# Optimization experiments

Measured on AMD Instinct MI355X. Metric: run time of the kernel, lower is better.

The kernel has to match this reference:

```python
import jax, jax.numpy as jnp
import numpy as np

P = 7            # pooling_size
SCALE = 1.0 / 16  # spatial_scale


def _roi_align(feat, tf):
    # feat: [B,C,T,H,W] (L2-normalized), tf: [N,7] = [b, x1, y1, t1, x2, y2, t2]
    # RoIAlignAvg with temporal pooled size == T (identity in time): bilinear
    # sample at each spatial bin center for every frame.
    H, W = feat.shape[-2], feat.shape[-1]
    b = tf[:, 0].astype(jnp.int32)
    x1, y1 = tf[:, 1] * SCALE, tf[:, 2] * SCALE
    x2, y2 = tf[:, 4] * SCALE, tf[:, 5] * SCALE
    bw = jnp.maximum(x2 - x1 + SCALE, 1e-3) / P
    bh = jnp.maximum(y2 - y1 + SCALE, 1e-3) / P
    ctr = jnp.arange(P, dtype=feat.dtype) + 0.5
    xs = jnp.clip(x1[:, None] + ctr * bw[:, None], 0.0, W - 1)  # [N,P]
    ys = jnp.clip(y1[:, None] + ctr * bh[:, None], 0.0, H - 1)  # [N,P]
    x0 = jnp.floor(xs); y0 = jnp.floor(ys)
    fx = xs - x0; fy = ys - y0
    x0i = x0.astype(jnp.int32); x1i = jnp.minimum(x0i + 1, W - 1)
    y0i = y0.astype(jnp.int32); y1i = jnp.minimum(y0i + 1, H - 1)

    def g(yi, xi):
        # advanced indices broadcast to [N,P,P]; result [N,P,P,C,T]
        return feat[b[:, None, None], :, :, yi[:, :, None], xi[:, None, :]]

    wy0 = (1 - fy)[:, :, None, None, None]; wy1 = fy[:, :, None, None, None]
    wx0 = (1 - fx)[:, None, :, None, None]; wx1 = fx[:, None, :, None, None]
    out = (wy0 * wx0 * g(y0i, x0i) + wy0 * wx1 * g(y0i, x1i)
           + wy1 * wx0 * g(y1i, x0i) + wy1 * wx1 * g(y1i, x1i))
    return jnp.transpose(out, (0, 3, 4, 1, 2))  # [N,C,T,P,P]


def _forward(base_feat, tubes, gt_rois, gt_tubes, conv_w, conv_b, w1, b1, w2, b2, wp, bp):
    B, C, T = base_feat.shape[:3]
    R = tubes.shape[1]
    # F.normalize(base_feat, p=2, dim=1)
    feat = base_feat / jnp.maximum(
        jnp.linalg.norm(base_feat, axis=1, keepdims=True), 1e-12)

    # --- ragged scatter: rois[b,i,t1:t2+1,1:] = tubes[b,i,[1,2,4,5]] ---
    f = jnp.arange(T)
    f_off = (f[None, :] + jnp.arange(B)[:, None] * T).astype(tubes.dtype)  # [B,T]
    t1 = tubes[..., 3].astype(jnp.int32)[..., None]
    t2 = tubes[..., 6].astype(jnp.int32)[..., None]
    mask = (f[None, None, :] >= t1) & (f[None, None, :] <= t2)  # [B,R,T]
    box = tubes[..., jnp.array([1, 2, 4, 5])]                   # [B,R,4]
    rois_box = jnp.where(mask[..., None], box[:, :, None, :],
                         jnp.zeros((), tubes.dtype))
    rois = jnp.concatenate(
        [jnp.broadcast_to(f_off[:, None, :, None], (B, R, T, 1)), rois_box], -1)

    # --- RoIAlign + AvgPool3d over T + head (eval mode: dropout = identity) ---
    pooled = _roi_align(feat, tubes.reshape(-1, 7))  # [N,C,T,P,P]
    pooled = pooled.mean(axis=2)                     # [N,C,P,P]
    x = jnp.einsum('nchw,oc->nohw', pooled, conv_w) + conv_b[None, :, None, None]
    x = x.reshape(x.shape[0], -1)                    # [N, C*P*P]
    x = jax.nn.relu(x @ w1 + b1)
    x = jax.nn.relu(x @ w2 + b2)
    bbox_pred = x @ wp + bp                          # [N, 4*T]
    return bbox_pred, pooled, rois


def setup_inputs() -> dict:
    B, R, T, C, HF, IMG = 4, 64, 16, 256, 14, 224
    ks = jax.random.split(jax.random.key(0), 16)
    base_feat = jax.random.normal(ks[0], (B, C, T, HF, HF), jnp.float32)
    x1 = jax.random.uniform(ks[1], (B, R), minval=0.0, maxval=IMG / 2)
    y1 = jax.random.uniform(ks[2], (B, R), minval=0.0, maxval=IMG / 2)
    x2 = jnp.minimum(x1 + jax.random.uniform(ks[3], (B, R), minval=16.0, maxval=IMG / 2), IMG - 1.0)
    y2 = jnp.minimum(y1 + jax.random.uniform(ks[4], (B, R), minval=16.0, maxval=IMG / 2), IMG - 1.0)
    tt = jax.random.randint(ks[5], (B, R, 2), 0, T)
    t1 = jnp.min(tt, -1).astype(jnp.float32)
    t2 = jnp.max(tt, -1).astype(jnp.float32)
    bidx = jnp.broadcast_to(jnp.arange(B)[:, None], (B, R)).astype(jnp.float32)
    tubes = jnp.stack([bidx, x1, y1, t1, x2, y2, t2], -1)
    s = 0.02
    return {
        'base_feat': base_feat,
        'tubes': tubes,
        'gt_rois': jax.random.normal(ks[6], (B, 10, T, 5), jnp.float32),
        'gt_tubes': jax.random.normal(ks[7], (B, 10, 7), jnp.float32),
        'conv_w': jax.random.normal(ks[8], (C, C), jnp.float32) * s,
        'conv_b': jnp.zeros((C,), jnp.float32),
        'w1': jax.random.normal(ks[9], (C * P * P, 2048), jnp.float32) * s,
        'b1': jnp.zeros((2048,), jnp.float32),
        'w2': jax.random.normal(ks[10], (2048, 512), jnp.float32) * s,
        'b2': jnp.zeros((512,), jnp.float32),
        'wp': jax.random.normal(ks[11], (512, 4 * T), jnp.float32) * s,
        'bp': jnp.zeros((4 * T,), jnp.float32),
    }


def reference(base_feat, tubes, gt_rois, gt_tubes, conv_w, conv_b, w1, b1, w2, b2, wp, bp):
    return _forward(base_feat, tubes, gt_rois, gt_tubes, conv_w, conv_b, w1, b1, w2, b2, wp, bp)
```

## Files before the change

### kernel.cpp

```cpp
#include <hip/hip_runtime.h>

#define HH 14
#define WW 14
#define HWSZ 196
#define TT 16
#define CC 256
#define BB 4
#define RR 64
#define NROI 256
#define PP 7
#define PP2 49

typedef short s4v __attribute__((ext_vector_type(4)));
typedef short s8v __attribute__((ext_vector_type(8)));
typedef float f4v __attribute__((ext_vector_type(4)));

__device__ inline ushort f2bf(float f) {
    union { float f; unsigned u; } v; v.f = f;
    unsigned r = v.u + 0x7fffu + ((v.u >> 16) & 1u);
    return (ushort)(r >> 16);
}
__device__ inline float bf2f(ushort u) {
    union { unsigned u; float f; } v; v.u = ((unsigned)u) << 16;
    return v.f;
}

__global__ void k_sumsq(const float* __restrict__ base, float* __restrict__ partial) {
    int blk = blockIdx.x;
    int bt = blk >> 3, cg = blk & 7;
    int hw = threadIdx.x;
    if (hw >= HWSZ) return;
    int b = bt >> 4, t = bt & 15;
    const float* p = base + ((size_t)(b * CC + cg * 32) * TT + t) * HWSZ + hw;
    float s = 0.f;
    #pragma unroll 8
    for (int c = 0; c < 32; ++c) {
        float v = p[(size_t)c * TT * HWSZ];
        s += v * v;
    }
    partial[cg * 12544 + bt * HWSZ + hw] = s;
}

__global__ void k_finish_inv(const float* __restrict__ partial, float* __restrict__ inv) {
    int j = blockIdx.x * 256 + threadIdx.x;
    if (j >= 12544) return;
    float s = 0.f;
    #pragma unroll
    for (int cg = 0; cg < 8; ++cg) s += partial[cg * 12544 + j];
    inv[j] = 1.0f / fmaxf(sqrtf(s), 1e-12f);
}

__global__ void k_tsum(const float* __restrict__ base, const float* __restrict__ inv,
                       float* __restrict__ tsum) {
    int bc = blockIdx.x;
    int hw = threadIdx.x;
    if (hw >= HWSZ) return;
    int b = bc >> 8;
    const float* p = base + (size_t)bc * TT * HWSZ + hw;
    const float* iv = inv + b * TT * HWSZ + hw;
    float s = 0.f;
    #pragma unroll
    for (int t = 0; t < TT; ++t) s += p[t * HWSZ] * iv[t * HWSZ];
    tsum[(size_t)bc * HWSZ + hw] = s;
}

__global__ void k_roialign(const float* __restrict__ tubes, const float* __restrict__ tsum,
                           float* __restrict__ pooled, float* __restrict__ pooledT,
                           float* __restrict__ rois) {
    __shared__ int sx0[PP], sx1[PP], sy0[PP], sy1[PP];
    __shared__ float sfx[PP], sfy[PP];
    __shared__ int sb;
    int n = blockIdx.x;
    int tid = threadIdx.x;
    if (tid < PP) {
        const float* tb = tubes + n * 7;
        float x1 = tb[1] * 0.0625f, y1 = tb[2] * 0.0625f;
        float x2 = tb[4] * 0.0625f, y2 = tb[5] * 0.0625f;
        float bw = fmaxf(x2 - x1 + 0.0625f, 0.001f) * (1.0f / PP);
        float bh = fmaxf(y2 - y1 + 0.0625f, 0.001f) * (1.0f / PP);
        float ctr = tid + 0.5f;
        float xs = fminf(fmaxf(x1 + ctr * bw, 0.f), (float)(WW - 1));
        float ys = fminf(fmaxf(y1 + ctr * bh, 0.f), (float)(HH - 1));
        float x0f = floorf(xs), y0f = floorf(ys);
        int x0 = (int)x0f, y0 = (int)y0f;
        sx0[tid] = x0; sx1[tid] = min(x0 + 1, WW - 1);
        sy0[tid] = y0; sy1[tid] = min(y0 + 1, HH - 1);
        sfx[tid] = xs - x0f; sfy[tid] = ys - y0f;
        if (tid == 0) sb = (int)tb[0];
    }
    if (tid < TT) {
        const float* tb = tubes + n * 7;
        int t1 = (int)tb[3], t2 = (int)tb[6];
        bool m = (tid >= t1) && (tid <= t2);
        int b = n >> 6;
        float* o = rois + ((size_t)n * TT + tid) * 5;
        o[0] = (float)(b * TT + tid);
        o[1] = m ? tb[1] : 0.f;
        o[2] = m ? tb[2] : 0.f;
        o[3] = m ? tb[4] : 0.f;
        o[4] = m ? tb[5] : 0.f;
    }
    __syncthreads();
    const float* tbase = tsum + (size_t)sb * CC * HWSZ;

    for (int idx = tid; idx < CC * PP2; idx += 256) {
        int c = idx / PP2, bin = idx - (idx / PP2) * PP2;
        int py = bin / PP, px = bin - (bin / PP) * PP;
        const float* tp = tbase + (size_t)c * HWSZ;
        float fx = sfx[px], fy = sfy[py];
        int y0 = sy0[py] * WW, y1 = sy1[py] * WW;
        float v00 = tp[y0 + sx0[px]];
        float v01 = tp[y0 + sx1[px]];
        float v10 = tp[y1 + sx0[px]];
        float v11 = tp[y1 + sx1[px]];
        float v = (1.f - fy) * ((1.f - fx) * v00 + fx * v01)
                + fy        * ((1.f - fx) * v10 + fx * v11);
        pooled[(size_t)n * CC * PP2 + idx] = v * (1.0f / TT);
    }
    for (int idx = tid; idx < PP2 * CC; idx += 256) {
        int bin = idx >> 8, c = idx & 255;
        int py = bin / PP, px = bin - (bin / PP) * PP;
        const float* tp = tbase + (size_t)c * HWSZ;
        float fx = sfx[px], fy = sfy[py];
        int y0 = sy0[py] * WW, y1 = sy1[py] * WW;
        float v00 = tp[y0 + sx0[px]];
        float v01 = tp[y0 + sx1[px]];
        float v10 = tp[y1 + sx0[px]];
        float v11 = tp[y1 + sx1[px]];
        float v = (1.f - fy) * ((1.f - fx) * v00 + fx * v01)
                + fy        * ((1.f - fx) * v10 + fx * v11);
        pooledT[((size_t)n * PP2 + bin) * CC + c] = v * (1.0f / TT);
    }
}

__global__ __launch_bounds__(512) void conv_mfma(const float* __restrict__ pooledT,
                                                 const float* __restrict__ conv_w,
                                                 const float* __restrict__ conv_b,
                                                 ushort* __restrict__ xb) {
    __shared__ __align__(16) ushort Ab[2][8192];
    __shared__ __align__(16) ushort Bres[8192];
    const int m0 = blockIdx.x * 256, o0 = blockIdx.y * 64;
    const int tid = threadIdx.x;
    const int lane = tid & 63, w = tid >> 6;
    const int wm = w & 3, wn = w >> 2;
    const int fr = lane & 15, fg = lane >> 4;

    for (int ii = tid; ii < 2048; ii += 512) {
        int o_l = ii >> 5, cq = ii & 31;
        const float* s = conv_w + (size_t)(o0 + o_l) * 256 + cq * 8;
        float4 v0 = *(const float4*)s;
        float4 v1 = *(const float4*)(s + 4);
        float vv[8] = {v0.x, v0.y, v0.z, v0.w, v1.x, v1.y, v1.z, v1.w};
        int dbase = (cq >> 2) * 2048 + (o_l >> 4) * 512 + (cq & 3) * 128 + (o_l & 15);
        #pragma unroll
        for (int jc = 0; jc < 8; ++jc) Bres[dbase + jc * 16] = f2bf(vv[jc]);
    }

    int ii0 = tid, ii1 = 512 + tid, ii2 = 1024 + tid, ii3 = 1536 + tid;
    const float* pA0 = pooledT + (size_t)(m0 + (ii0 >> 3)) * 256 + (ii0 & 7) * 4;
    const float* pA1 = pooledT + (size_t)(m0 + (ii1 >> 3)) * 256 + (ii1 & 7) * 4;
    const float* pA2 = pooledT + (size_t)(m0 + (ii2 >> 3)) * 256 + (ii2 & 7) * 4;
    const float* pA3 = pooledT + (size_t)(m0 + (ii3 >> 3)) * 256 + (ii3 & 7) * 4;
#define CDOFF(ii) (((ii >> 3) >> 4) * 512 + ((ii & 7) >> 1) * 128 + ((ii >> 3) & 15) * 8 + (ii & 1) * 4)
    const int do0 = CDOFF(ii0), do1 = CDOFF(ii1), do2 = CDOFF(ii2), do3 = CDOFF(ii3);
#undef CDOFF
    float4 a0_, a1_, a2_, a3_;
#define CONV_LOAD(t) do { a0_ = *(const float4*)(pA0 + (t) * 32); \
                          a1_ = *(const float4*)(pA1 + (t) * 32); \
                          a2_ = *(const float4*)(pA2 + (t) * 32); \
                          a3_ = *(const float4*)(pA3 + (t) * 32); } while (0)
#define W4(dst, v) do { s4v _u; _u[0]=(short)f2bf((v).x); _u[1]=(short)f2bf((v).y); \
                        _u[2]=(short)f2bf((v).z); _u[3]=(short)f2bf((v).w); \
                        *(s4v*)(dst) = _u; } while (0)
#define CONV_WRITE(buf) do { W4(Ab[buf] + do0, a0_); W4(Ab[buf] + do1, a1_); \
                             W4(Ab[buf] + do2, a2_); W4(Ab[buf] + do3, a3_); } while (0)

    CONV_LOAD(0);
    CONV_WRITE(0);
    __syncthreads();

    const int aoff = wm * 2048 + fg * 128 + fr * 8;
    f4v acc[4][2];
    #pragma unroll
    for (int i = 0; i < 4; ++i)
        #pragma unroll
        for (int j = 0; j < 2; ++j) acc[i][j] = (f4v){0.f, 0.f, 0.f, 0.f};

    for (int t = 0; t < 8; ++t) {
        if (t < 7) CONV_LOAD(t + 1);
        const ushort* A = Ab[t & 1];
        s8v a0 = *(const s8v*)(A + aoff);
        s8v a1 = *(const s8v*)(A + aoff + 512);
        s8v a2 = *(const s8v*)(A + aoff + 1024);
        s8v a3 = *(const s8v*)(A + aoff + 1536);
        unsigned bbase = (unsigned)(size_t)(&Bres[0]) + t * 4096 + wn * 2048 + fg * 256 + fr * 2;
        s4v bl0, bh0, bl1, bh1;
        asm volatile("ds_read_b64_tr_b16 %0, %2\n\t"
                     "ds_read_b64_tr_b16 %1, %2 offset:128"
                     : "=v"(bl0), "=v"(bh0) : "v"(bbase));
        asm volatile("ds_read_b64_tr_b16 %0, %2 offset:1024\n\t"
                     "ds_read_b64_tr_b16 %1, %2 offset:1152"
                     : "=v"(bl1), "=v"(bh1) : "v"(bbase));
        asm volatile("s_waitcnt lgkmcnt(0)" ::: "memory");
        __builtin_amdgcn_sched_barrier(0);
        s8v b0, b1;
        b0[0] = bl0[0]; b0[1] = bl0[1]; b0[2] = bl0[2]; b0[3] = bl0[3];
        b0[4] = bh0[0]; b0[5] = bh0[1]; b0[6] = bh0[2]; b0[7] = bh0[3];
        b1[0] = bl1[0]; b1[1] = bl1[1]; b1[2] = bl1[2]; b1[3] = bl1[3];
        b1[4] = bh1[0]; b1[5] = bh1[1]; b1[6] = bh1[2]; b1[7] = bh1[3];
        acc[0][0] = __builtin_amdgcn_mfma_f32_16x16x32_bf16(a0, b0, acc[0][0], 0, 0, 0);
        acc[0][1] = __builtin_amdgcn_mfma_f32_16x16x32_bf16(a0, b1, acc[0][1], 0, 0, 0);
        acc[1][0] = __builtin_amdgcn_mfma_f32_16x16x32_bf16(a1, b0, acc[1][0], 0, 0, 0);
        acc[1][1] = __builtin_amdgcn_mfma_f32_16x16x32_bf16(a1, b1, acc[1][1], 0, 0, 0);
        acc[2][0] = __builtin_amdgcn_mfma_f32_16x16x32_bf16(a2, b0, acc[2][0], 0, 0, 0);
        acc[2][1] = __builtin_amdgcn_mfma_f32_16x16x32_bf16(a2, b1, acc[2][1], 0, 0, 0);
        acc[3][0] = __builtin_amdgcn_mfma_f32_16x16x32_bf16(a3, b0, acc[3][0], 0, 0, 0);
        acc[3][1] = __builtin_amdgcn_mfma_f32_16x16x32_bf16(a3, b1, acc[3][1], 0, 0, 0);
        if (t < 7) CONV_WRITE((t + 1) & 1);
        __syncthreads();
    }
#undef CONV_LOAD
#undef CONV_WRITE
#undef W4

    #pragma unroll
    for (int ni = 0; ni < 2; ++ni) {
        int o = o0 + wn * 32 + ni * 16 + fr;
        float cb = conv_b[o];
        int obase = (o >> 5) * 8192 + (((o >> 3) & 3)) * 128 + (o & 7);
        #pragma unroll
        for (int mi = 0; mi < 4; ++mi)
            #pragma unroll
            for (int i = 0; i < 4; ++i) {
                int gm = m0 + wm * 64 + mi * 16 + fg * 4 + i;
                int n = gm / 49, hw = gm - n * 49;
                xb[(size_t)hw * 65536 + obase + (n >> 4) * 512 + (n & 15) * 8]
                    = f2bf(acc[mi][ni][i] + cb);
            }
    }
}

__global__ __launch_bounds__(512) void fc1_mfma(const ushort* __restrict__ xb,
                                                const float* __restrict__ w1,
                                                ushort* __restrict__ partb) {
    __shared__ __align__(16) ushort Ab[4][8192];
    __shared__ __align__(16) ushort Bbf[2][2048];
    const int s = blockIdx.x, nblk = blockIdx.y;
    const int n0 = nblk * 64;
    const int k0 = s * 1568;
    const int tid = threadIdx.x;
    const int lane = tid & 63, w = tid >> 6;
    const int wm = w & 3, wn = w >> 2;
    const int fr = lane & 15, fg = lane >> 4;

    const ushort* gA = xb + (size_t)s * 49 * 8192;
    const int slot0 = tid, slot1 = 512 + tid;

    const int kr = (w >> 2) * 16 + (lane >> 2);
    const int bnb = w & 3, bnq = lane & 3;
    const int ncol = n0 + bnb * 16 + bnq * 4;
    const int bw_u = bnb * 512 + kr * 16 + bnq * 4;

    const int aoff = wm * 2048 + fg * 128 + fr * 8;
    f4v acc[4][2];
    #pragma unroll
    for (int i = 0; i < 4; ++i)
        #pragma unroll
        for (int j = 0; j < 2; ++j) acc[i][j] = (f4v){0.f, 0.f, 0.f, 0.f};

#define STAGE_A(buf, kg) do {                                                                   \
    ushort* _d = Ab[buf];                                                                       \
    __builtin_amdgcn_global_load_lds(                                                           \
        (const __attribute__((address_space(1))) void*)(gA + (size_t)(kg) * 8192 + slot0 * 8),  \
        (__attribute__((address_space(3))) void*)(_d + slot0 * 8), 16, 0, 0);                   \
    __builtin_amdgcn_global_load_lds(                                                           \
        (const __attribute__((address_space(1))) void*)(gA + (size_t)(kg) * 8192 + slot1 * 8),  \
        (__attribute__((address_space(3))) void*)(_d + slot1 * 8), 16, 0, 0);                   \
} while (0)
#define GBP(t) (*(const float4*)(w1 +                                                           \
    (size_t)(((unsigned)(k0 + (t) * 32 + kr) & 255u) * 49 +                                     \
             ((unsigned)(k0 + (t) * 32 + kr) >> 8)) * 2048 + ncol))
#define BWRITE(buf, rb) do {                                                                    \
    s4v _u; _u[0] = (short)f2bf((rb).x); _u[1] = (short)f2bf((rb).y);                           \
    _u[2] = (short)f2bf((rb).z); _u[3] = (short)f2bf((rb).w);                                   \
    *(s4v*)&Bbf[buf][bw_u] = _u;                                                                \
} while (0)

    float4 rb0, rb1, rb2, rb3;
    STAGE_A(0, 0);
    STAGE_A(1, 1);
    rb0 = GBP(0); rb1 = GBP(1); rb2 = GBP(2); rb3 = GBP(3);
    BWRITE(0, rb0);
    __builtin_amdgcn_sched_barrier(0);
    asm volatile("s_waitcnt vmcnt(3) lgkmcnt(0)" ::: "memory");
    __builtin_amdgcn_s_barrier();
    __builtin_amdgcn_sched_barrier(0);

#define FC1_BODY(t, rbL, rbU) do {                                                              \
    int kg2 = (t) + 2 > 48 ? 48 : (t) + 2;                                                      \
    int kg4 = (t) + 4 > 48 ? 48 : (t) + 4;                                                      \
    STAGE_A(((t) + 2) & 3, kg2);                                                                \
    __builtin_amdgcn_sched_barrier(0);                                                          \
    rbL = GBP(kg4);                                                                             \
    __builtin_amdgcn_sched_barrier(0);                                                          \
    const ushort* _A = Ab[(t) & 3];                                                             \
    s8v _a0 = *(const s8v*)(_A + aoff);                                                         \
    s8v _a1 = *(const s8v*)(_A + aoff + 512);                                                   \
    s8v _a2 = *(const s8v*)(_A + aoff + 1024);                                                  \
    s8v _a3 = *(const s8v*)(_A + aoff + 1536);                                                  \
    unsigned _bb = (unsigned)(size_t)(&Bbf[(t) & 1][0]) + wn * 2048 + fg * 256 + fr * 2;        \
    s4v _bl0, _bh0, _bl1, _bh1;                                                                 \
    asm volatile("ds_read_b64_tr_b16 %0, %2\n\t"                                                \
                 "ds_read_b64_tr_b16 %1, %2 offset:128"                                         \
                 : "=v"(_bl0), "=v"(_bh0) : "v"(_bb));                                          \
    asm volatile("ds_read_b64_tr_b16 %0, %2 offset:1024\n\t"                                    \
                 "ds_read_b64_tr_b16 %1, %2 offset:1152"                                        \
                 : "=v"(_bl1), "=v"(_bh1) : "v"(_bb));                                          \
    asm volatile("s_waitcnt lgkmcnt(0)" ::: "memory");                                          \
    __builtin_amdgcn_sched_barrier(0);                                                          \
    s8v _b0, _b1;                                                                               \
    _b0[0]=_bl0[0]; _b0[1]=_bl0[1]; _b0[2]=_bl0[2]; _b0[3]=_bl0[3];                             \
    _b0[4]=_bh0[0]; _b0[5]=_bh0[1]; _b0[6]=_bh0[2]; _b0[7]=_bh0[3];                             \
    _b1[0]=_bl1[0]; _b1[1]=_bl1[1]; _b1[2]=_bl1[2]; _b1[3]=_bl1[3];                             \
    _b1[4]=_bh1[0]; _b1[5]=_bh1[1]; _b1[6]=_bh1[2]; _b1[7]=_bh1[3];                             \
    acc[0][0] = __builtin_amdgcn_mfma_f32_16x16x32_bf16(_a0, _b0, acc[0][0], 0, 0, 0);          \
    acc[0][1] = __builtin_amdgcn_mfma_f32_16x16x32_bf16(_a0, _b1, acc[0][1], 0, 0, 0);          \
    acc[1][0] = __builtin_amdgcn_mfma_f32_16x16x32_bf16(_a1, _b0, acc[1][0], 0, 0, 0);          \
    acc[1][1] = __builtin_amdgcn_mfma_f32_16x16x32_bf16(_a1, _b1, acc[1][1], 0, 0, 0);          \
    acc[2][0] = __builtin_amdgcn_mfma_f32_16x16x32_bf16(_a2, _b0, acc[2][0], 0, 0, 0);          \
    acc[2][1] = __builtin_amdgcn_mfma_f32_16x16x32_bf16(_a2, _b1, acc[2][1], 0, 0, 0);          \
    acc[3][0] = __builtin_amdgcn_mfma_f32_16x16x32_bf16(_a3, _b0, acc[3][0], 0, 0, 0);          \
    acc[3][1] = __builtin_amdgcn_mfma_f32_16x16x32_bf16(_a3, _b1, acc[3][1], 0, 0, 0);          \
    BWRITE(((t) + 1) & 1, rbU);                                                                 \
    __builtin_amdgcn_sched_barrier(0);                                                          \
    asm volatile("s_waitcnt vmcnt(4) lgkmcnt(0)" ::: "memory");                                 \
    __builtin_amdgcn_s_barrier();                                                               \
    __builtin_amdgcn_sched_barrier(0);                                                          \
} while (0)

    for (int tb = 0; tb < 48; tb += 4) {
        FC1_BODY(tb + 0, rb0, rb1);
        FC1_BODY(tb + 1, rb1, rb2);
        FC1_BODY(tb + 2, rb2, rb3);
        FC1_BODY(tb + 3, rb3, rb0);
    }

    {
        const ushort* _A = Ab[0];
        s8v _a0 = *(const s8v*)(_A + aoff);
        s8v _a1 = *(const s8v*)(_A + aoff + 512);
        s8v _a2 = *(const s8v*)(_A + aoff + 1024);
        s8v _a3 = *(const s8v*)(_A + aoff + 1536);
        unsigned _bb = (unsigned)(size_t)(&Bbf[0][0]) + wn * 2048 + fg * 256 + fr * 2;
        s4v _bl0, _bh0, _bl1, _bh1;
        asm volatile("ds_read_b64_tr_b16 %0, %2\n\t"
                     "ds_read_b64_tr_b16 %1, %2 offset:128"
                     : "=v"(_bl0), "=v"(_bh0) : "v"(_bb));
        asm volatile("ds_read_b64_tr_b16 %0, %2 offset:1024\n\t"
                     "ds_read_b64_tr_b16 %1, %2 offset:1152"
                     : "=v"(_bl1), "=v"(_bh1) : "v"(_bb));
        asm volatile("s_waitcnt lgkmcnt(0)" ::: "memory");
        __builtin_amdgcn_sched_barrier(0);
        s8v _b0, _b1;
        _b0[0]=_bl0[0]; _b0[1]=_bl0[1]; _b0[2]=_bl0[2]; _b0[3]=_bl0[3];
        _b0[4]=_bh0[0]; _b0[5]=_bh0[1]; _b0[6]=_bh0[2]; _b0[7]=_bh0[3];
        _b1[0]=_bl1[0]; _b1[1]=_bl1[1]; _b1[2]=_bl1[2]; _b1[3]=_bl1[3];
        _b1[4]=_bh1[0]; _b1[5]=_bh1[1]; _b1[6]=_bh1[2]; _b1[7]=_bh1[3];
        acc[0][0] = __builtin_amdgcn_mfma_f32_16x16x32_bf16(_a0, _b0, acc[0][0], 0, 0, 0);
        acc[0][1] = __builtin_amdgcn_mfma_f32_16x16x32_bf16(_a0, _b1, acc[0][1], 0, 0, 0);
        acc[1][0] = __builtin_amdgcn_mfma_f32_16x16x32_bf16(_a1, _b0, acc[1][0], 0, 0, 0);
        acc[1][1] = __builtin_amdgcn_mfma_f32_16x16x32_bf16(_a1, _b1, acc[1][1], 0, 0, 0);
        acc[2][0] = __builtin_amdgcn_mfma_f32_16x16x32_bf16(_a2, _b0, acc[2][0], 0, 0, 0);
        acc[2][1] = __builtin_amdgcn_mfma_f32_16x16x32_bf16(_a2, _b1, acc[2][1], 0, 0, 0);
        acc[3][0] = __builtin_amdgcn_mfma_f32_16x16x32_bf16(_a3, _b0, acc[3][0], 0, 0, 0);
        acc[3][1] = __builtin_amdgcn_mfma_f32_16x16x32_bf16(_a3, _b1, acc[3][1], 0, 0, 0);
    }
#undef FC1_BODY
#undef STAGE_A
#undef GBP
#undef BWRITE

    ushort* dst = partb + (size_t)s * 524288 + n0 + wn * 32 + fr;
    #pragma unroll
    for (int mi = 0; mi < 4; ++mi)
        #pragma unroll
        for (int ni = 0; ni < 2; ++ni)
            #pragma unroll
            for (int i = 0; i < 4; ++i) {
                int row = wm * 64 + mi * 16 + fg * 4 + i;
                dst[(size_t)row * 2048 + ni * 16] = f2bf(acc[mi][ni][i]);
            }
}

__global__ void k_reduce_bf(const ushort* __restrict__ part, const float* __restrict__ bias,
                            ushort* __restrict__ h1b) {
    int idx = blockIdx.x * 256 + threadIdx.x;
    if (idx >= 65536) return;
    int m = idx >> 8;
    int ko = idx & 255;
    int kbase = ko * 8;
    float s[8];
    #pragma unroll
    for (int j = 0; j < 8; ++j) s[j] = bias[kbase + j];
    #pragma unroll
    for (int i = 0; i < 8; ++i) {
        s8v v = *(const s8v*)(part + (size_t)i * 524288 + (size_t)m * 2048 + kbase);
        #pragma unroll
        for (int j = 0; j < 8; ++j) s[j] += bf2f((ushort)v[j]);
    }
    ushort o[8];
    #pragma unroll
    for (int j = 0; j < 8; ++j) o[j] = f2bf(fmaxf(s[j], 0.f));
    size_t dst = (size_t)(ko >> 2) * 8192 + (m >> 4) * 512 + (ko & 3) * 128 + (m & 15) * 8;
    *(s8v*)(h1b + dst) = *(s8v*)o;
}

__global__ __launch_bounds__(512) void fc2_mfma(const ushort* __restrict__ h1b,
                                                const float* __restrict__ w2,
                                                ushort* __restrict__ partb2) {
    __shared__ __align__(16) ushort Bbf[2][2048];
    const int s = blockIdx.x, nblk = blockIdx.y;
    const int n0 = nblk * 64;
    const int k0 = s * 256;
    const int tid = threadIdx.x;
    const int lane = tid & 63, w = tid >> 6;
    const int wm = w & 3, wn = w >> 2;
    const int fr = lane & 15, fg = lane >> 4;

    const ushort* gA = h1b + (size_t)s * 8 * 8192;

    const int kr = (w >> 2) * 16 + (lane >> 2);
    const int bnb = w & 3, bnq = lane & 3;
    const int ncol = n0 + bnb * 16 + bnq * 4;
    const int bw_u = bnb * 512 + kr * 16 + bnq * 4;

    const int aoff = wm * 2048 + fg * 128 + fr * 8;
    f4v acc[4][2];
    #pragma unroll
    for (int i = 0; i < 4; ++i)
        #pragma unroll
        for (int j = 0; j < 2; ++j) acc[i][j] = (f4v){0.f, 0.f, 0.f, 0.f};

#define GBP2(t) (*(const float4*)(w2 + (size_t)(k0 + (t) * 32 + kr) * 512 + ncol))
#define BWRITE2(buf, rb) do {                                                                   \
    s4v _u; _u[0] = (short)f2bf((rb).x); _u[1] = (short)f2bf((rb).y);                           \
    _u[2] = (short)f2bf((rb).z); _u[3] = (short)f2bf((rb).w);                                   \
    *(s4v*)&Bbf[buf][bw_u] = _u;                                                                \
} while (0)

    s8v aA0, aA1, aA2, aA3, aB0, aB1, aB2, aB3;
    float4 rb0, rb1, rb2, rb3;

    aA0 = *(const s8v*)(gA + aoff);
    aA1 = *(const s8v*)(gA + aoff + 512);
    aA2 = *(const s8v*)(gA + aoff + 1024);
    aA3 = *(const s8v*)(gA + aoff + 1536);
    rb0 = GBP2(0); rb1 = GBP2(1); rb2 = GBP2(2); rb3 = GBP2(3);
    BWRITE2(0, rb0);
    __syncthreads();

#define FC2_BODY(t, rbL, rbU, aC0, aC1, aC2, aC3, aN0, aN1, aN2, aN3) do {                      \
    int kg1 = (t) + 1 > 7 ? 7 : (t) + 1;                                                        \
    int kg4 = (t) + 4 > 7 ? 7 : (t) + 4;                                                        \
    const ushort* _gn = gA + (size_t)kg1 * 8192;                                                \
    aN0 = *(const s8v*)(_gn + aoff);                                                            \
    aN1 = *(const s8v*)(_gn + aoff + 512);                                                      \
    aN2 = *(const s8v*)(_gn + aoff + 1024);                                                     \
    aN3 = *(const s8v*)(_gn + aoff + 1536);                                                     \
    rbL = GBP2(kg4);                                                                            \
    unsigned _bb = (unsigned)(size_t)(&Bbf[(t) & 1][0]) + wn * 2048 + fg * 256 + fr * 2;        \
    s4v _bl0, _bh0, _bl1, _bh1;                                                                 \
    asm volatile("ds_read_b64_tr_b16 %0, %2\n\t"                                                \
                 "ds_read_b64_tr_b16 %1, %2 offset:128"                                         \
                 : "=v"(_bl0), "=v"(_bh0) : "v"(_bb));                                          \
    asm volatile("ds_read_b64_tr_b16 %0, %2 offset:1024\n\t"                                    \
                 "ds_read_b64_tr_b16 %1, %2 offset:1152"                                        \
                 : "=v"(_bl1), "=v"(_bh1) : "v"(_bb));                                          \
    asm volatile("s_waitcnt lgkmcnt(0)" ::: "memory");                                          \
    __builtin_amdgcn_sched_barrier(0);                                                          \
    s8v _b0, _b1;                                                                               \
    _b0[0]=_bl0[0]; _b0[1]=_bl0[1]; _b0[2]=_bl0[2]; _b0[3]=_bl0[3];                             \
    _b0[4]=_bh0[0]; _b0[5]=_bh0[1]; _b0[6]=_bh0[2]; _b0[7]=_bh0[3];                             \
    _b1[0]=_bl1[0]; _b1[1]=_bl1[1]; _b1[2]=_bl1[2]; _b1[3]=_bl1[3];                             \
    _b1[4]=_bh1[0]; _b1[5]=_bh1[1]; _b1[6]=_bh1[2]; _b1[7]=_bh1[3];                             \
    acc[0][0] = __builtin_amdgcn_mfma_f32_16x16x32_bf16(aC0, _b0, acc[0][0], 0, 0, 0);          \
    acc[0][1] = __builtin_amdgcn_mfma_f32_16x16x32_bf16(aC0, _b1, acc[0][1], 0, 0, 0);          \
    acc[1][0] = __builtin_amdgcn_mfma_f32_16x16x32_bf16(aC1, _b0, acc[1][0], 0, 0, 0);          \
    acc[1][1] = __builtin_amdgcn_mfma_f32_16x16x32_bf16(aC1, _b1, acc[1][1], 0, 0, 0);          \
    acc[2][0] = __builtin_amdgcn_mfma_f32_16x16x32_bf16(aC2, _b0, acc[2][0], 0, 0, 0);          \
    acc[2][1] = __builtin_amdgcn_mfma_f32_16x16x32_bf16(aC2, _b1, acc[2][1], 0, 0, 0);          \
    acc[3][0] = __builtin_amdgcn_mfma_f32_16x16x32_bf16(aC3, _b0, acc[3][0], 0, 0, 0);          \
    acc[3][1] = __builtin_amdgcn_mfma_f32_16x16x32_bf16(aC3, _b1, acc[3][1], 0, 0, 0);          \
    BWRITE2(((t) + 1) & 1, rbU);                                                                \
    __syncthreads();                                                                            \
} while (0)

    FC2_BODY(0, rb0, rb1, aA0, aA1, aA2, aA3, aB0, aB1, aB2, aB3);
    FC2_BODY(1, rb1, rb2, aB0, aB1, aB2, aB3, aA0, aA1, aA2, aA3);
    FC2_BODY(2, rb2, rb3, aA0, aA1, aA2, aA3, aB0, aB1, aB2, aB3);
    FC2_BODY(3, rb3, rb0, aB0, aB1, aB2, aB3, aA0, aA1, aA2, aA3);
    FC2_BODY(4, rb0, rb1, aA0, aA1, aA2, aA3, aB0, aB1, aB2, aB3);
    FC2_BODY(5, rb1, rb2, aB0, aB1, aB2, aB3, aA0, aA1, aA2, aA3);
    FC2_BODY(6, rb2, rb3, aA0, aA1, aA2, aA3, aB0, aB1, aB2, aB3);

    {
        unsigned _bb = (unsigned)(size_t)(&Bbf[1][0]) + wn * 2048 + fg * 256 + fr * 2;
        s4v _bl0, _bh0, _bl1, _bh1;
        asm volatile("ds_read_b64_tr_b16 %0, %2\n\t"
                     "ds_read_b64_tr_b16 %1, %2 offset:128"
                     : "=v"(_bl0), "=v"(_bh0) : "v"(_bb));
        asm volatile("ds_read_b64_tr_b16 %0, %2 offset:1024\n\t"
                     "ds_read_b64_tr_b16 %1, %2 offset:1152"
                     : "=v"(_bl1), "=v"(_bh1) : "v"(_bb));
        asm volatile("s_waitcnt lgkmcnt(0)" ::: "memory");
        __builtin_amdgcn_sched_barrier(0);
        s8v _b0, _b1;
        _b0[0]=_bl0[0]; _b0[1]=_bl0[1]; _b0[2]=_bl0[2]; _b0[3]=_bl0[3];
        _b0[4]=_bh0[0]; _b0[5]=_bh0[1]; _b0[6]=_bh0[2]; _b0[7]=_bh0[3];
        _b1[0]=_bl1[0]; _b1[1]=_bl1[1]; _b1[2]=_bl1[2]; _b1[3]=_bl1[3];
        _b1[4]=_bh1[0]; _b1[5]=_bh1[1]; _b1[6]=_bh1[2]; _b1[7]=_bh1[3];
        acc[0][0] = __builtin_amdgcn_mfma_f32_16x16x32_bf16(aB0, _b0, acc[0][0], 0, 0, 0);
        acc[0][1] = __builtin_amdgcn_mfma_f32_16x16x32_bf16(aB0, _b1, acc[0][1], 0, 0, 0);
        acc[1][0] = __builtin_amdgcn_mfma_f32_16x16x32_bf16(aB1, _b0, acc[1][0], 0, 0, 0);
        acc[1][1] = __builtin_amdgcn_mfma_f32_16x16x32_bf16(aB1, _b1, acc[1][1], 0, 0, 0);
        acc[2][0] = __builtin_amdgcn_mfma_f32_16x16x32_bf16(aB2, _b0, acc[2][0], 0, 0, 0);
        acc[2][1] = __builtin_amdgcn_mfma_f32_16x16x32_bf16(aB2, _b1, acc[2][1], 0, 0, 0);
        acc[3][0] = __builtin_amdgcn_mfma_f32_16x16x32_bf16(aB3, _b0, acc[3][0], 0, 0, 0);
        acc[3][1] = __builtin_amdgcn_mfma_f32_16x16x32_bf16(aB3, _b1, acc[3][1], 0, 0, 0);
    }
#undef FC2_BODY
#undef GBP2
#undef BWRITE2

    ushort* dst = partb2 + (size_t)s * 131072 + n0 + wn * 32 + fr;
    #pragma unroll
    for (int mi = 0; mi < 4; ++mi)
        #pragma unroll
        for (int ni = 0; ni < 2; ++ni)
            #pragma unroll
            for (int i = 0; i < 4; ++i) {
                int row = wm * 64 + mi * 16 + fg * 4 + i;
                dst[(size_t)row * 512 + ni * 16] = f2bf(acc[mi][ni][i]);
            }
}

__global__ void k_reduce_bf2(const ushort* __restrict__ part, const float* __restrict__ bias,
                             float* __restrict__ h2) {
    int idx = blockIdx.x * 256 + threadIdx.x;
    if (idx >= 16384) return;
    int m = idx >> 6;
    int no = idx & 63;
    int nbase = no * 8;
    float s[8];
    #pragma unroll
    for (int j = 0; j < 8; ++j) s[j] = bias[nbase + j];
    #pragma unroll
    for (int i = 0; i < 8; ++i) {
        s8v v = *(const s8v*)(part + (size_t)i * 131072 + (size_t)m * 512 + nbase);
        #pragma unroll
        for (int j = 0; j < 8; ++j) s[j] += bf2f((ushort)v[j]);
    }
    float* o = h2 + (size_t)m * 512 + nbase;
    #pragma unroll
    for (int j = 0; j < 8; ++j) o[j] = fmaxf(s[j], 0.f);
}

__global__ __launch_bounds__(256) void fc3_small(const float* __restrict__ h2,
                                                 const float* __restrict__ wp,
                                                 const float* __restrict__ bp,
                                                 float* __restrict__ bbox) {
    __shared__ float sh2[8][512];
    int blk = blockIdx.x;
    int tid = threadIdx.x;
    int n = tid & 63;
    int mr = tid >> 6;
    int m0 = blk * 8;
    for (int i = tid; i < 8 * 512; i += 256)
        sh2[i >> 9][i & 511] = h2[(size_t)(m0 + (i >> 9)) * 512 + (i & 511)];
    __syncthreads();
    float b = bp[n];
    float acc0 = b, acc1 = b;
    for (int k = 0; k < 512; ++k) {
        float wv = wp[k * 64 + n];
        acc0 += sh2[mr][k] * wv;
        acc1 += sh2[mr + 4][k] * wv;
    }
    bbox[(size_t)(m0 + mr) * 64 + n] = acc0;
    bbox[(size_t)(m0 + mr + 4) * 64 + n] = acc1;
}

extern "C" void kernel_launch(void* const* d_in, const int* in_sizes, int n_in,
                              void* d_out, int out_size, void* d_ws, size_t ws_size,
                              hipStream_t stream) {
    const float* base   = (const float*)d_in[0];
    const float* tubes  = (const float*)d_in[1];
    const float* conv_w = (const float*)d_in[4];
    const float* conv_b = (const float*)d_in[5];
    const float* w1     = (const float*)d_in[6];
    const float* b1     = (const float*)d_in[7];
    const float* w2     = (const float*)d_in[8];
    const float* b2     = (const float*)d_in[9];
    const float* wp     = (const float*)d_in[10];
    const float* bp     = (const float*)d_in[11];

    float* out    = (float*)d_out;
    float* bbox   = out;
    float* pooled = out + 16384;
    float* rois   = out + 16384 + 3211264;

    float* ws      = (float*)d_ws;
    float* inv     = ws;
    float* partial = ws + 12544;
    float* tsum    = ws + 112896;
    float* pooledT = ws + 313600;
    ushort* xb     = (ushort*)(ws + 3524864);
    ushort* h1b    = (ushort*)(ws + 6736128);
    float* h2      = ws + 7260416;
    float* part    = ws + 7391488;
    ushort* partb  = (ushort*)part;
    ushort* partb2 = (ushort*)(part + 2097152);

    k_sumsq<<<BB * TT * 8, 256, 0, stream>>>(base, partial);
    k_finish_inv<<<49, 256, 0, stream>>>(partial, inv);
    k_tsum<<<BB * CC, 256, 0, stream>>>(base, inv, tsum);
    k_roialign<<<NROI, 256, 0, stream>>>(tubes, tsum, pooled, pooledT, rois);

    conv_mfma<<<dim3(49, 4), 512, 0, stream>>>(pooledT, conv_w, conv_b, xb);

    fc1_mfma<<<dim3(8, 32), 512, 0, stream>>>(xb, w1, partb);
    k_reduce_bf<<<256, 256, 0, stream>>>(partb, b1, h1b);

    fc2_mfma<<<dim3(8, 8), 512, 0, stream>>>(h1b, w2, partb2);
    k_reduce_bf2<<<64, 256, 0, stream>>>(partb2, b2, h2);

    fc3_small<<<32, 256, 0, stream>>>(h2, wp, bp, bbox);
}
```

Baseline: 123.1 us.

## Fuse normalization finish and split-K reductions into consumer kernels

Removes three small kernels: the inverse-norm finish is folded into k_tsum, the fc1 split-K reduction with bias and ReLU is folded into the fc2 A-operand loads, and the fc2 reduction is folded into fc3's shared-memory staging. The aim is to cut launch overhead and the intermediate global round trips. In exchange, each fc2 block now re-reads eight bf16 partial slices per A fragment, repeated across the 8 N-blocks. k_tsum also recomputes the norm for every channel, which adds redundant global traffic and ALU work inside the fc2 inner loop.

```diff
diff --git a/kernel.cpp b/kernel.cpp
--- a/kernel.cpp
+++ b/kernel.cpp
@@ -41,26 +41,23 @@
     partial[cg * 12544 + bt * HWSZ + hw] = s;
 }
 
-__global__ void k_finish_inv(const float* __restrict__ partial, float* __restrict__ inv) {
-    int j = blockIdx.x * 256 + threadIdx.x;
-    if (j >= 12544) return;
-    float s = 0.f;
-    #pragma unroll
-    for (int cg = 0; cg < 8; ++cg) s += partial[cg * 12544 + j];
-    inv[j] = 1.0f / fmaxf(sqrtf(s), 1e-12f);
-}
-
-__global__ void k_tsum(const float* __restrict__ base, const float* __restrict__ inv,
+__global__ void k_tsum(const float* __restrict__ base, const float* __restrict__ partial,
                        float* __restrict__ tsum) {
     int bc = blockIdx.x;
     int hw = threadIdx.x;
     if (hw >= HWSZ) return;
     int b = bc >> 8;
     const float* p = base + (size_t)bc * TT * HWSZ + hw;
-    const float* iv = inv + b * TT * HWSZ + hw;
     float s = 0.f;
     #pragma unroll
-    for (int t = 0; t < TT; ++t) s += p[t * HWSZ] * iv[t * HWSZ];
+    for (int t = 0; t < TT; ++t) {
+        int bt = b * TT + t;
+        float ss = 0.f;
+        #pragma unroll
+        for (int cg = 0; cg < 8; ++cg) ss += partial[cg * 12544 + bt * HWSZ + hw];
+        float iv = 1.0f / fmaxf(sqrtf(ss), 1e-12f);
+        s += p[t * HWSZ] * iv;
+    }
     tsum[(size_t)bc * HWSZ + hw] = s;
 }
 
@@ -392,30 +389,26 @@
             }
 }
 
-__global__ void k_reduce_bf(const ushort* __restrict__ part, const float* __restrict__ bias,
-                            ushort* __restrict__ h1b) {
-    int idx = blockIdx.x * 256 + threadIdx.x;
-    if (idx >= 65536) return;
-    int m = idx >> 8;
-    int ko = idx & 255;
-    int kbase = ko * 8;
+__device__ inline s8v frag_reduce(const ushort* __restrict__ partb,
+                                  const float* __restrict__ b1,
+                                  int rowoff, int kglob) {
     float s[8];
     #pragma unroll
-    for (int j = 0; j < 8; ++j) s[j] = bias[kbase + j];
-    #pragma unroll
-    for (int i = 0; i < 8; ++i) {
-        s8v v = *(const s8v*)(part + (size_t)i * 524288 + (size_t)m * 2048 + kbase);
+    for (int j = 0; j < 8; ++j) s[j] = b1[kglob + j];
+    #pragma unroll
+    for (int sp = 0; sp < 8; ++sp) {
+        s8v v = *(const s8v*)(partb + (size_t)sp * 524288 + rowoff + kglob);
         #pragma unroll
         for (int j = 0; j < 8; ++j) s[j] += bf2f((ushort)v[j]);
     }
-    ushort o[8];
-    #pragma unroll
-    for (int j = 0; j < 8; ++j) o[j] = f2bf(fmaxf(s[j], 0.f));
-    size_t dst = (size_t)(ko >> 2) * 8192 + (m >> 4) * 512 + (ko & 3) * 128 + (m & 15) * 8;
-    *(s8v*)(h1b + dst) = *(s8v*)o;
-}
-
-__global__ __launch_bounds__(512) void fc2_mfma(const ushort* __restrict__ h1b,
+    s8v o;
+    #pragma unroll
+    for (int j = 0; j < 8; ++j) o[j] = (short)f2bf(fmaxf(s[j], 0.f));
+    return o;
+}
+
+__global__ __launch_bounds__(512) void fc2_mfma(const ushort* __restrict__ partb,
+                                                const float* __restrict__ b1,
                                                 const float* __restrict__ w2,
                                                 ushort* __restrict__ partb2) {
     __shared__ __align__(16) ushort Bbf[2][2048];
@@ -427,14 +420,14 @@
     const int wm = w & 3, wn = w >> 2;
     const int fr = lane & 15, fg = lane >> 4;
 
-    const ushort* gA = h1b + (size_t)s * 8 * 8192;
-
     const int kr = (w >> 2) * 16 + (lane >> 2);
     const int bnb = w & 3, bnq = lane & 3;
     const int ncol = n0 + bnb * 16 + bnq * 4;
     const int bw_u = bnb * 512 + kr * 16 + bnq * 4;
 
-    const int aoff = wm * 2048 + fg * 128 + fr * 8;
+    const int row0 = (wm * 64 + fr) * 2048;
+    const int kf = fg * 8;
+
     f4v acc[4][2];
     #pragma unroll
     for (int i = 0; i < 4; ++i)
@@ -447,26 +440,26 @@
     _u[2] = (short)f2bf((rb).z); _u[3] = (short)f2bf((rb).w);                                   \
     *(s4v*)&Bbf[buf][bw_u] = _u;                                                                \
 } while (0)
+#define LOAD_A(t, d0, d1, d2, d3) do {                                                          \
+    int _kg = (t) > 7 ? 7 : (t);                                                                \
+    int _kk = k0 + _kg * 32 + kf;                                                               \
+    d0 = frag_reduce(partb, b1, row0,             _kk);                                         \
+    d1 = frag_reduce(partb, b1, row0 + 32768,     _kk);                                         \
+    d2 = frag_reduce(partb, b1, row0 + 65536,     _kk);                                         \
+    d3 = frag_reduce(partb, b1, row0 + 98304,     _kk);                                         \
+} while (0)
 
     s8v aA0, aA1, aA2, aA3, aB0, aB1, aB2, aB3;
     float4 rb0, rb1, rb2, rb3;
 
-    aA0 = *(const s8v*)(gA + aoff);
-    aA1 = *(const s8v*)(gA + aoff + 512);
-    aA2 = *(const s8v*)(gA + aoff + 1024);
-    aA3 = *(const s8v*)(gA + aoff + 1536);
+    LOAD_A(0, aA0, aA1, aA2, aA3);
     rb0 = GBP2(0); rb1 = GBP2(1); rb2 = GBP2(2); rb3 = GBP2(3);
     BWRITE2(0, rb0);
     __syncthreads();
 
 #define FC2_BODY(t, rbL, rbU, aC0, aC1, aC2, aC3, aN0, aN1, aN2, aN3) do {                      \
-    int kg1 = (t) + 1 > 7 ? 7 : (t) + 1;                                                        \
     int kg4 = (t) + 4 > 7 ? 7 : (t) + 4;                                                        \
-    const ushort* _gn = gA + (size_t)kg1 * 8192;                                                \
-    aN0 = *(const s8v*)(_gn + aoff);                                                            \
-    aN1 = *(const s8v*)(_gn + aoff + 512);                                                      \
-    aN2 = *(const s8v*)(_gn + aoff + 1024);                                                     \
-    aN3 = *(const s8v*)(_gn + aoff + 1536);                                                     \
+    LOAD_A((t) + 1, aN0, aN1, aN2, aN3);                                                        \
     rbL = GBP2(kg4);                                                                            \
     unsigned _bb = (unsigned)(size_t)(&Bbf[(t) & 1][0]) + wn * 2048 + fg * 256 + fr * 2;        \
     s4v _bl0, _bh0, _bl1, _bh1;                                                                 \
@@ -529,6 +522,7 @@
         acc[3][1] = __builtin_amdgcn_mfma_f32_16x16x32_bf16(aB3, _b1, acc[3][1], 0, 0, 0);
     }
 #undef FC2_BODY
+#undef LOAD_A
 #undef GBP2
 #undef BWRITE2
 
@@ -544,40 +538,33 @@
             }
 }
 
-__global__ void k_reduce_bf2(const ushort* __restrict__ part, const float* __restrict__ bias,
-                             float* __restrict__ h2) {
-    int idx = blockIdx.x * 256 + threadIdx.x;
-    if (idx >= 16384) return;
-    int m = idx >> 6;
-    int no = idx & 63;
-    int nbase = no * 8;
-    float s[8];
-    #pragma unroll
-    for (int j = 0; j < 8; ++j) s[j] = bias[nbase + j];
-    #pragma unroll
-    for (int i = 0; i < 8; ++i) {
-        s8v v = *(const s8v*)(part + (size_t)i * 131072 + (size_t)m * 512 + nbase);
-        #pragma unroll
-        for (int j = 0; j < 8; ++j) s[j] += bf2f((ushort)v[j]);
-    }
-    float* o = h2 + (size_t)m * 512 + nbase;
-    #pragma unroll
-    for (int j = 0; j < 8; ++j) o[j] = fmaxf(s[j], 0.f);
-}
-
-__global__ __launch_bounds__(256) void fc3_small(const float* __restrict__ h2,
+__global__ __launch_bounds__(256) void fc3_small(const ushort* __restrict__ partb2,
+                                                 const float* __restrict__ b2,
                                                  const float* __restrict__ wp,
                                                  const float* __restrict__ bp,
                                                  float* __restrict__ bbox) {
     __shared__ float sh2[8][512];
     int blk = blockIdx.x;
     int tid = threadIdx.x;
+    int m0 = blk * 8;
+    for (int i = tid; i < 8 * 64; i += 256) {
+        int r = i >> 6, ko = i & 63;
+        int kb = ko * 8;
+        float s[8];
+        #pragma unroll
+        for (int j = 0; j < 8; ++j) s[j] = b2[kb + j];
+        #pragma unroll
+        for (int sp = 0; sp < 8; ++sp) {
+            s8v v = *(const s8v*)(partb2 + (size_t)sp * 131072 + (size_t)(m0 + r) * 512 + kb);
+            #pragma unroll
+            for (int j = 0; j < 8; ++j) s[j] += bf2f((ushort)v[j]);
+        }
+        #pragma unroll
+        for (int j = 0; j < 8; ++j) sh2[r][kb + j] = fmaxf(s[j], 0.f);
+    }
+    __syncthreads();
     int n = tid & 63;
     int mr = tid >> 6;
-    int m0 = blk * 8;
-    for (int i = tid; i < 8 * 512; i += 256)
-        sh2[i >> 9][i & 511] = h2[(size_t)(m0 + (i >> 9)) * 512 + (i & 511)];
-    __syncthreads();
     float b = bp[n];
     float acc0 = b, acc1 = b;
     for (int k = 0; k < 512; ++k) {
@@ -609,29 +596,23 @@
     float* rois   = out + 16384 + 3211264;
 
     float* ws      = (float*)d_ws;
-    float* inv     = ws;
     float* partial = ws + 12544;
     float* tsum    = ws + 112896;
     float* pooledT = ws + 313600;
     ushort* xb     = (ushort*)(ws + 3524864);
-    ushort* h1b    = (ushort*)(ws + 6736128);
-    float* h2      = ws + 7260416;
     float* part    = ws + 7391488;
     ushort* partb  = (ushort*)part;
     ushort* partb2 = (ushort*)(part + 2097152);
 
     k_sumsq<<<BB * TT * 8, 256, 0, stream>>>(base, partial);
-    k_finish_inv<<<49, 256, 0, stream>>>(partial, inv);
-    k_tsum<<<BB * CC, 256, 0, stream>>>(base, inv, tsum);
+    k_tsum<<<BB * CC, 256, 0, stream>>>(base, partial, tsum);
     k_roialign<<<NROI, 256, 0, stream>>>(tubes, tsum, pooled, pooledT, rois);
 
     conv_mfma<<<dim3(49, 4), 512, 0, stream>>>(pooledT, conv_w, conv_b, xb);
 
     fc1_mfma<<<dim3(8, 32), 512, 0, stream>>>(xb, w1, partb);
-    k_reduce_bf<<<256, 256, 0, stream>>>(partb, b1, h1b);
-
-    fc2_mfma<<<dim3(8, 8), 512, 0, stream>>>(h1b, w2, partb2);
-    k_reduce_bf2<<<64, 256, 0, stream>>>(partb2, b2, h2);
-
-    fc3_small<<<32, 256, 0, stream>>>(h2, wp, bp, bbox);
-}
+
+    fc2_mfma<<<dim3(8, 8), 512, 0, stream>>>(partb, b1, w2, partb2);
+
+    fc3_small<<<32, 256, 0, stream>>>(partb2, b2, wp, bp, bbox);
+}
```

After: 180.5 us. 46.7% more time.
